# Kernel tuning notes

Measured on AMD Instinct MI355X. Metric: run time of the kernel, lower is better.

## Reference

```python
import jax, jax.numpy as jnp
import numpy as np

B, L, D, O = 4, 256, 512, 128

def setup_inputs() -> dict:
    key = jax.random.key(0)
    k1, k2, k3, k4, k5, k6 = jax.random.split(key, 6)
    return {
        "x1": jax.random.normal(k1, (B, L, D), jnp.float32),
        "x2": jax.random.normal(k2, (B, L, D), jnp.float32),
        "bw": jax.random.uniform(k3, (2,), jnp.float32),
        "W_bil": jax.random.normal(k4, (O, D + 1, D + 1), jnp.float32) * 0.02,
        "W_lin": jax.random.normal(k5, (2 * D, O), jnp.float32) * 0.02,
        "b_lin": jax.random.normal(k6, (O,), jnp.float32) * 0.02,
    }

def reference(x1, x2, bw, W_bil, W_lin, b_lin):
    bwn = jax.nn.softmax(bw)
    d1 = x1.shape[-1]
    # Bilinear with bias_x/bias_y: append ones column to x1 and x2.
    ones1 = jnp.ones((*x1.shape[:2], 1), x1.dtype)
    ones2 = jnp.ones((*x2.shape[:2], 1), x2.dtype)
    x1b = jnp.concatenate([x1, ones1], axis=-1)  # [B, L1, D+1]
    x2b = jnp.concatenate([x2, ones2], axis=-1)  # [B, L2, D+1]
    # einsum 'bxi,oij,byj->boxy' then permute(0,2,3,1) -> bxyo
    bilinear_logits = jnp.einsum('bxi,oij,byj->bxyo', x1b, W_bil, x2b)
    # linear over concat([x1 expanded, x2 expanded]) == split-weight broadcast sum
    lin1 = x1 @ W_lin[:d1]   # [B, L1, O]
    lin2 = x2 @ W_lin[d1:]   # [B, L2, O]
    linear_logits = lin1[:, :, None, :] + lin2[:, None, :, :] + b_lin  # [B, L1, L2, O]
    return bwn[0] * bilinear_logits + bwn[1] * linear_logits
```

## Files before the change

kernel.cpp:

```cpp
#include <hip/hip_runtime.h>


#define LL 256
#define DD 512
#define OO 128
#define BB 4
#define WB_OI 263169
#define WB_R512 262656

typedef __attribute__((ext_vector_type(8))) short  short8;
typedef __attribute__((ext_vector_type(8))) unsigned short us8;
typedef __attribute__((ext_vector_type(4))) unsigned short us4;
typedef __attribute__((ext_vector_type(4))) float  f32x4;

__device__ __forceinline__ unsigned short f2bf(float f) {
    unsigned int u = __builtin_bit_cast(unsigned int, f);
    u = (u + 0x7FFFu + ((u >> 16) & 1u)) >> 16;
    return (unsigned short)u;
}
__device__ __forceinline__ float bf2f(unsigned short s) {
    return __builtin_bit_cast(float, (unsigned int)s << 16);
}
__device__ __forceinline__ void load_lds16(const void* g, void* l) {
    __builtin_amdgcn_global_load_lds(
        (const __attribute__((address_space(1))) unsigned int*)g,
        (__attribute__((address_space(3))) unsigned int*)l, 16, 0, 0);
}

__global__ __launch_bounds__(256) void cast2_kernel(
    const float* __restrict__ x1, const float* __restrict__ x2,
    unsigned short* __restrict__ x1b, unsigned short* __restrict__ x2b)
{
    int i = blockIdx.x * 256 + threadIdx.x;
    const float* s; unsigned short* d; int j;
    if (i < 131072) { s = x1; d = x1b; j = i; }
    else            { s = x2; d = x2b; j = i - 131072; }
    float4 v = ((const float4*)s)[j];
    us4 u; u.x = f2bf(v.x); u.y = f2bf(v.y); u.z = f2bf(v.z); u.w = f2bf(v.w);
    *(us4*)(d + (size_t)j * 4) = u;
}

__global__ __launch_bounds__(256) void prepw_kernel(
    const float* __restrict__ Wb, const float* __restrict__ bw,
    unsigned short* __restrict__ Wb16)
{
    const int t = threadIdx.x;
    const int row = blockIdx.x * 4 + (t >> 6);
    const int o = row >> 9, i = row & 511;
    const int l = t & 63;
    const float e0 = __expf(bw[0]), e1 = __expf(bw[1]);
    const float bwn0 = e0 / (e0 + e1);
    const float* src = Wb + (size_t)o * WB_OI + (size_t)i * 513;
    unsigned short* dst = Wb16 + (size_t)row * 512;
    float v[8];
    #pragma unroll
    for (int e = 0; e < 8; ++e) v[e] = src[e * 64 + l];
    #pragma unroll
    for (int e = 0; e < 8; ++e) dst[e * 64 + l] = f2bf(bwn0 * v[e]);
}

__global__ __launch_bounds__(256) void prep512_kernel(
    const float* __restrict__ Wb, float* __restrict__ W512T)
{
    int idx = blockIdx.x * 256 + threadIdx.x;
    if (idx < 513 * 128) {
        const int o = idx & 127, j = idx >> 7;
        W512T[idx] = Wb[(size_t)o * WB_OI + WB_R512 + j];
    }
}

__global__ __launch_bounds__(128) void u512_kernel(
    const float* __restrict__ x2, const float* __restrict__ W512T,
    const float* __restrict__ W_lin, const float* __restrict__ b_lin,
    const float* __restrict__ bw, float* __restrict__ u512buf)
{
    __shared__ float xs[DD];
    const int by = blockIdx.x;
    const int o  = threadIdx.x;
    const float* xr = x2 + (size_t)by * DD;
    for (int j = o; j < DD; j += 128) xs[j] = xr[j];
    __syncthreads();
    float s1 = W512T[512 * 128 + o];
    float s2 = b_lin[o];
    #pragma unroll 4
    for (int j = 0; j < DD; ++j) {
        s1 += xs[j] * W512T[j * 128 + o];
        s2 += xs[j] * W_lin[(size_t)(DD + j) * OO + o];
    }
    const float e0 = __expf(bw[0]), e1 = __expf(bw[1]);
    const float bwn0 = e0 / (e0 + e1), bwn1 = e1 / (e0 + e1);
    u512buf[(size_t)by * OO + o] = bwn0 * s1 + bwn1 * s2;
}

__global__ __launch_bounds__(256) void passA_kernel(
    const unsigned short* __restrict__ x2b, const unsigned short* __restrict__ Wb16,
    const float* __restrict__ W_bil, const float* __restrict__ W_lin,
    const float* __restrict__ bw, unsigned short* __restrict__ Up)
{
    __shared__ __align__(16) char smem[33280];
    unsigned short* As0 = (unsigned short*)smem;
    unsigned short* Bs0 = (unsigned short*)(smem + 8192);
    unsigned short* As1 = (unsigned short*)(smem + 16384);
    unsigned short* Bs1 = (unsigned short*)(smem + 24576);
    unsigned short* Cs  = (unsigned short*)smem;
    float* corr = (float*)(smem + 32768);

    const int t = threadIdx.x, w = t >> 6, l = t & 63;
    const int ib = blockIdx.x * 128;
    const int yg = blockIdx.y * 128;
    const int o  = blockIdx.z;
    const int wy = w & 1, wx = w >> 1;

    f32x4 acc[4][4] = {};
    const unsigned short* Wo16 = Wb16 + (size_t)o * DD * DD;

    const int rb0 = w * 32;
    const int rr  = l >> 2;
    const int kof = (l & 3) * 8;

#define STAGE_A(ASP, BSP, K0) do {                                              \
    _Pragma("unroll")                                                           \
    for (int q = 0; q < 2; ++q) {                                               \
        const int rb = rb0 + q * 16, rrow = rb + rr, ko = (K0) + kof;           \
        load_lds16(x2b  + (size_t)(yg + rrow) * DD + ko, (ASP) + rb * 32);      \
        load_lds16(Wo16 + (size_t)(ib + rrow) * DD + ko, (BSP) + rb * 32);      \
    } } while (0)

    STAGE_A(As0, Bs0, 0);
    __syncthreads();

    const int mrow = wy * 64 + (l & 15);
    const int ncol = wx * 64 + (l & 15);
    const int kg = (l >> 4) * 8;

    #pragma unroll 2
    for (int kt = 0; kt < 16; ++kt) {
        const int cur = kt & 1;
        unsigned short* Asr = cur ? As1 : As0;
        unsigned short* Bsr = cur ? Bs1 : Bs0;
        unsigned short* Asn = cur ? As0 : As1;
        unsigned short* Bsn = cur ? Bs0 : Bs1;
        if (kt < 15) STAGE_A(Asn, Bsn, (kt + 1) * 32);
        short8 af[4], bfr[4];
        #pragma unroll
        for (int mt = 0; mt < 4; ++mt) af[mt]  = *(const short8*)(Asr + (mrow + mt * 16) * 32 + kg);
        #pragma unroll
        for (int nt = 0; nt < 4; ++nt) bfr[nt] = *(const short8*)(Bsr + (ncol + nt * 16) * 32 + kg);
        #pragma unroll
        for (int mt = 0; mt < 4; ++mt)
            #pragma unroll
            for (int nt = 0; nt < 4; ++nt)
                acc[mt][nt] = __builtin_amdgcn_mfma_f32_16x16x32_bf16(af[mt], bfr[nt], acc[mt][nt], 0, 0, 0);
        __syncthreads();
    }
#undef STAGE_A

    const float e0 = __expf(bw[0]), e1 = __expf(bw[1]);
    const float bwn0 = e0 / (e0 + e1), bwn1 = e1 / (e0 + e1);
    if (t < 128) {
        const int ig = ib + t;
        corr[t] = bwn1 * W_lin[(size_t)ig * OO + o]
                + bwn0 * W_bil[(size_t)o * WB_OI + (size_t)ig * 513 + 512];
    }
    #pragma unroll
    for (int half = 0; half < 2; ++half) {
        if (wy == half) {
            #pragma unroll
            for (int mt = 0; mt < 4; ++mt) {
                const int yl = mt * 16 + ((l >> 4) << 2);
                #pragma unroll
                for (int nt = 0; nt < 4; ++nt) {
                    const int ic = wx * 64 + nt * 16 + (l & 15);
                    #pragma unroll
                    for (int r = 0; r < 4; ++r)
                        Cs[(yl + r) * 136 + ic] = f2bf(acc[mt][nt][r]);
                }
            }
        }
        __syncthreads();
        #pragma unroll
        for (int p = 0; p < 4; ++p) {
            const int yl = p * 16 + (t >> 4);
            const int i0 = (t & 15) * 8;
            short8 v = *(const short8*)(Cs + yl * 136 + i0);
            us8 uo;
            #pragma unroll
            for (int e = 0; e < 8; ++e)
                uo[e] = f2bf(bf2f((unsigned short)v[e]) + corr[i0 + e]);
            *(us8*)(Up + ((size_t)(yg + half * 64 + yl) * OO + o) * DD + ib + i0) = uo;
        }
        __syncthreads();
    }
}

__global__ __launch_bounds__(256) void passB_kernel(
    const unsigned short* __restrict__ x1b, const unsigned short* __restrict__ Up,
    const float* __restrict__ u512buf, float* __restrict__ out)
{
    __shared__ __align__(16) char smem[33280];
    unsigned short* As0 = (unsigned short*)smem;
    unsigned short* Bs0 = (unsigned short*)(smem + 8192);
    unsigned short* As1 = (unsigned short*)(smem + 16384);
    unsigned short* Bs1 = (unsigned short*)(smem + 24576);
    float* u5 = (float*)(smem + 32768);

    const int t = threadIdx.x, w = t >> 6, l = t & 63;
    const int xb = blockIdx.x * 128;
    const int yg = blockIdx.y;
    const int bb = yg >> 8, y = yg & 255;
    const int wy = w & 1, wx = w >> 1;
    if (t < 128) u5[t] = u512buf[(size_t)yg * OO + t];

    f32x4 acc[4][4] = {};

    const int rb0 = w * 32;
    const int rr  = l >> 2;
    const int kof = (l & 3) * 8;

#define STAGE_B(ASP, BSP, K0) do {                                                   \
    _Pragma("unroll")                                                                \
    for (int q = 0; q < 2; ++q) {                                                    \
        const int rb = rb0 + q * 16, rrow = rb + rr, ko = (K0) + kof;                \
        load_lds16(x1b + (size_t)(bb * LL + xb + rrow) * DD + ko, (ASP) + rb * 32);  \
        load_lds16(Up  + (size_t)(yg * OO + rrow) * DD + ko,      (BSP) + rb * 32);  \
    } } while (0)

    STAGE_B(As0, Bs0, 0);
    __syncthreads();

    const int mrow = wy * 64 + (l & 15);
    const int ncol = wx * 64 + (l & 15);
    const int kg = (l >> 4) * 8;

    #pragma unroll 2
    for (int kt = 0; kt < 16; ++kt) {
        const int cur = kt & 1;
        unsigned short* Asr = cur ? As1 : As0;
        unsigned short* Bsr = cur ? Bs1 : Bs0;
        unsigned short* Asn = cur ? As0 : As1;
        unsigned short* Bsn = cur ? Bs0 : Bs1;
        if (kt < 15) STAGE_B(Asn, Bsn, (kt + 1) * 32);
        short8 af[4], bfr[4];
        #pragma unroll
        for (int mt = 0; mt < 4; ++mt) af[mt]  = *(const short8*)(Asr + (mrow + mt * 16) * 32 + kg);
        #pragma unroll
        for (int nt = 0; nt < 4; ++nt) bfr[nt] = *(const short8*)(Bsr + (ncol + nt * 16) * 32 + kg);
        #pragma unroll
        for (int mt = 0; mt < 4; ++mt)
            #pragma unroll
            for (int nt = 0; nt < 4; ++nt)
                acc[mt][nt] = __builtin_amdgcn_mfma_f32_16x16x32_bf16(af[mt], bfr[nt], acc[mt][nt], 0, 0, 0);
        __syncthreads();
    }
#undef STAGE_B

    #pragma unroll
    for (int mt = 0; mt < 4; ++mt) {
        const int xr = wy * 64 + mt * 16 + ((l >> 4) << 2);
        #pragma unroll
        for (int nt = 0; nt < 4; ++nt) {
            const int oc = wx * 64 + nt * 16 + (l & 15);
            const float c = u5[oc];
            #pragma unroll
            for (int r = 0; r < 4; ++r)
                out[((size_t)(bb * LL + xb + xr + r) * LL + y) * OO + oc] = acc[mt][nt][r] + c;
        }
    }
}

extern "C" void kernel_launch(void* const* d_in, const int* in_sizes, int n_in,
                              void* d_out, int out_size, void* d_ws, size_t ws_size,
                              hipStream_t stream)
{
    const float* x1    = (const float*)d_in[0];
    const float* x2    = (const float*)d_in[1];
    const float* bw    = (const float*)d_in[2];
    const float* W_bil = (const float*)d_in[3];
    const float* W_lin = (const float*)d_in[4];
    const float* b_lin = (const float*)d_in[5];
    float* out = (float*)d_out;

    char* ws = (char*)d_ws;
    unsigned short* x1b16 = (unsigned short*)ws;
    unsigned short* x2b16 = (unsigned short*)(ws + (1u << 20));
    float*          u512b = (float*)(ws + (2u << 20));
    float*          W512T = (float*)(ws + (2u << 20) + (512u << 10));
    unsigned short* Wb16  = (unsigned short*)(ws + (3u << 20));
    unsigned short* Up    = (unsigned short*)(ws + (3u << 20) + ((size_t)128 * 512 * 512 * 2));

    cast2_kernel<<<1024, 256, 0, stream>>>(x1, x2, x1b16, x2b16);
    prepw_kernel<<<16384, 256, 0, stream>>>(W_bil, bw, Wb16);
    prep512_kernel<<<257, 256, 0, stream>>>(W_bil, W512T);
    u512_kernel<<<BB * LL, 128, 0, stream>>>(x2, W512T, W_lin, b_lin, bw, u512b);

    passA_kernel<<<dim3(4, 8, OO), 256, 0, stream>>>(x2b16, Wb16, W_bil, W_lin, bw, Up);
    passB_kernel<<<dim3(2, BB * LL), 256, 0, stream>>>(x1b16, Up, u512b, out);
}
```

Measured before the change: 479.8 us.

## Swizzle LDS tile layout, add occupancy hints, merge cast and W512 prep kernels

XOR-swizzles the 16-byte chunk placement in the LDS tiles of both GEMM passes, on the global_load_lds write side and the MFMA fragment read side, to cut LDS bank conflicts. Adds a min-blocks-per-CU hint of 4 to passA and passB so the compiler limits register use. Merges the input cast kernel and the W512 transpose kernel into one launch to save a kernel launch. The occupancy hint could force register spilling.

Measured after the change: 452.3 us. -5.7%, faster.

```diff
diff --git a/kernel.cpp b/kernel.cpp
--- a/kernel.cpp
+++ b/kernel.cpp
@@ -27,17 +27,27 @@
         (__attribute__((address_space(3))) unsigned int*)l, 16, 0, 0);
 }
 
-__global__ __launch_bounds__(256) void cast2_kernel(
+__global__ __launch_bounds__(256) void castprep_kernel(
     const float* __restrict__ x1, const float* __restrict__ x2,
-    unsigned short* __restrict__ x1b, unsigned short* __restrict__ x2b)
-{
-    int i = blockIdx.x * 256 + threadIdx.x;
-    const float* s; unsigned short* d; int j;
-    if (i < 131072) { s = x1; d = x1b; j = i; }
-    else            { s = x2; d = x2b; j = i - 131072; }
-    float4 v = ((const float4*)s)[j];
-    us4 u; u.x = f2bf(v.x); u.y = f2bf(v.y); u.z = f2bf(v.z); u.w = f2bf(v.w);
-    *(us4*)(d + (size_t)j * 4) = u;
+    unsigned short* __restrict__ x1b, unsigned short* __restrict__ x2b,
+    const float* __restrict__ Wb, float* __restrict__ W512T)
+{
+    const int bid = blockIdx.x;
+    if (bid < 1024) {
+        int i = bid * 256 + threadIdx.x;
+        const float* s; unsigned short* d; int j;
+        if (i < 131072) { s = x1; d = x1b; j = i; }
+        else            { s = x2; d = x2b; j = i - 131072; }
+        float4 v = ((const float4*)s)[j];
+        us4 u; u.x = f2bf(v.x); u.y = f2bf(v.y); u.z = f2bf(v.z); u.w = f2bf(v.w);
+        *(us4*)(d + (size_t)j * 4) = u;
+    } else {
+        int idx = (bid - 1024) * 256 + threadIdx.x;
+        if (idx < 513 * 128) {
+            const int o = idx & 127, j = idx >> 7;
+            W512T[idx] = Wb[(size_t)o * WB_OI + WB_R512 + j];
+        }
+    }
 }
 
 __global__ __launch_bounds__(256) void prepw_kernel(
@@ -57,16 +67,6 @@
     for (int e = 0; e < 8; ++e) v[e] = src[e * 64 + l];
     #pragma unroll
     for (int e = 0; e < 8; ++e) dst[e * 64 + l] = f2bf(bwn0 * v[e]);
-}
-
-__global__ __launch_bounds__(256) void prep512_kernel(
-    const float* __restrict__ Wb, float* __restrict__ W512T)
-{
-    int idx = blockIdx.x * 256 + threadIdx.x;
-    if (idx < 513 * 128) {
-        const int o = idx & 127, j = idx >> 7;
-        W512T[idx] = Wb[(size_t)o * WB_OI + WB_R512 + j];
-    }
 }
 
 __global__ __launch_bounds__(128) void u512_kernel(
@@ -92,7 +92,7 @@
     u512buf[(size_t)by * OO + o] = bwn0 * s1 + bwn1 * s2;
 }
 
-__global__ __launch_bounds__(256) void passA_kernel(
+__global__ __launch_bounds__(256, 4) void passA_kernel(
     const unsigned short* __restrict__ x2b, const unsigned short* __restrict__ Wb16,
     const float* __restrict__ W_bil, const float* __restrict__ W_lin,
     const float* __restrict__ bw, unsigned short* __restrict__ Up)
@@ -116,7 +116,7 @@
 
     const int rb0 = w * 32;
     const int rr  = l >> 2;
-    const int kof = (l & 3) * 8;
+    const int kof = ((l & 3) ^ ((l >> 3) & 3)) * 8;
 
 #define STAGE_A(ASP, BSP, K0) do {                                              \
     _Pragma("unroll")                                                           \
@@ -131,7 +131,7 @@
 
     const int mrow = wy * 64 + (l & 15);
     const int ncol = wx * 64 + (l & 15);
-    const int kg = (l >> 4) * 8;
+    const int psel = ((l >> 4) ^ ((l >> 1) & 3)) * 8;
 
     #pragma unroll 2
     for (int kt = 0; kt < 16; ++kt) {
@@ -143,9 +143,9 @@
         if (kt < 15) STAGE_A(Asn, Bsn, (kt + 1) * 32);
         short8 af[4], bfr[4];
         #pragma unroll
-        for (int mt = 0; mt < 4; ++mt) af[mt]  = *(const short8*)(Asr + (mrow + mt * 16) * 32 + kg);
-        #pragma unroll
-        for (int nt = 0; nt < 4; ++nt) bfr[nt] = *(const short8*)(Bsr + (ncol + nt * 16) * 32 + kg);
+        for (int mt = 0; mt < 4; ++mt) af[mt]  = *(const short8*)(Asr + (mrow + mt * 16) * 32 + psel);
+        #pragma unroll
+        for (int nt = 0; nt < 4; ++nt) bfr[nt] = *(const short8*)(Bsr + (ncol + nt * 16) * 32 + psel);
         #pragma unroll
         for (int mt = 0; mt < 4; ++mt)
             #pragma unroll
@@ -193,7 +193,7 @@
     }
 }
 
-__global__ __launch_bounds__(256) void passB_kernel(
+__global__ __launch_bounds__(256, 4) void passB_kernel(
     const unsigned short* __restrict__ x1b, const unsigned short* __restrict__ Up,
     const float* __restrict__ u512buf, float* __restrict__ out)
 {
@@ -215,7 +215,7 @@
 
     const int rb0 = w * 32;
     const int rr  = l >> 2;
-    const int kof = (l & 3) * 8;
+    const int kof = ((l & 3) ^ ((l >> 3) & 3)) * 8;
 
 #define STAGE_B(ASP, BSP, K0) do {                                                   \
     _Pragma("unroll")                                                                \
@@ -230,7 +230,7 @@
 
     const int mrow = wy * 64 + (l & 15);
     const int ncol = wx * 64 + (l & 15);
-    const int kg = (l >> 4) * 8;
+    const int psel = ((l >> 4) ^ ((l >> 1) & 3)) * 8;
 
     #pragma unroll 2
     for (int kt = 0; kt < 16; ++kt) {
@@ -242,9 +242,9 @@
         if (kt < 15) STAGE_B(Asn, Bsn, (kt + 1) * 32);
         short8 af[4], bfr[4];
         #pragma unroll
-        for (int mt = 0; mt < 4; ++mt) af[mt]  = *(const short8*)(Asr + (mrow + mt * 16) * 32 + kg);
-        #pragma unroll
-        for (int nt = 0; nt < 4; ++nt) bfr[nt] = *(const short8*)(Bsr + (ncol + nt * 16) * 32 + kg);
+        for (int mt = 0; mt < 4; ++mt) af[mt]  = *(const short8*)(Asr + (mrow + mt * 16) * 32 + psel);
+        #pragma unroll
+        for (int nt = 0; nt < 4; ++nt) bfr[nt] = *(const short8*)(Bsr + (ncol + nt * 16) * 32 + psel);
         #pragma unroll
         for (int mt = 0; mt < 4; ++mt)
             #pragma unroll
@@ -288,9 +288,8 @@
     unsigned short* Wb16  = (unsigned short*)(ws + (3u << 20));
     unsigned short* Up    = (unsigned short*)(ws + (3u << 20) + ((size_t)128 * 512 * 512 * 2));
 
-    cast2_kernel<<<1024, 256, 0, stream>>>(x1, x2, x1b16, x2b16);
+    castprep_kernel<<<1281, 256, 0, stream>>>(x1, x2, x1b16, x2b16, W_bil, W512T);
     prepw_kernel<<<16384, 256, 0, stream>>>(W_bil, bw, Wb16);
-    prep512_kernel<<<257, 256, 0, stream>>>(W_bil, W512T);
     u512_kernel<<<BB * LL, 128, 0, stream>>>(x2, W512T, W_lin, b_lin, bw, u512b);
 
     passA_kernel<<<dim3(4, 8, OO), 256, 0, stream>>>(x2b16, Wb16, W_bil, W_lin, bw, Up);
```
